# Optimization experiments

Measured on AMD Instinct MI355X. Metric: run time of the kernel, lower is better.

Reference implementation:

```python
import jax, jax.numpy as jnp
import numpy as np

OUTPUT_SIZE = 65
THRESHOLD = 0.2
EPS = 1e-6


def setup_inputs() -> dict:
    key = jax.random.key(0)
    x = jax.random.normal(key, (64, 4, 512), dtype=jnp.float32)
    return {"x": x}


def _valid_mask(x):
    # True from first nonzero to last nonzero along L, per (n, c); all False if row is all-zero.
    N, C, L = x.shape
    nz = x != 0
    any_nz = nz.any(axis=2, keepdims=True)            # [N, C, 1]
    first = jnp.argmax(nz, axis=2)                    # [N, C]
    last = (L - 1) - jnp.argmax(nz[:, :, ::-1], axis=2)
    idx = jnp.arange(L)
    mask = (idx[None, None, :] >= first[:, :, None]) & (idx[None, None, :] <= last[:, :, None])
    return mask & any_nz                              # [N, C, L] bool


def reference(x):
    N, C, L = x.shape
    mask = _valid_mask(x)
    mf = mask.astype(x.dtype)
    cnt = jnp.clip(mf.sum(axis=2), 1, None)           # [N, C]
    mean = (x * mf).sum(axis=2) / cnt                 # [N, C]
    var = (((x * mf - mean[..., None]) ** 2) * mf).sum(axis=2) / cnt
    std = jnp.sqrt(var)                               # [N, C]
    x_norm = (x - mean[..., None]) / jnp.clip(std, EPS, None)[..., None]
    x_norm = jnp.where(mask, x_norm, jnp.zeros((), x.dtype))  # [N, C, L]
    # Recurrence plot: cdist on 1-d points == |x_i - x_j|, thresholded.
    dist = jnp.abs(x_norm[..., :, None] - x_norm[..., None, :])  # [N, C, L, L]
    rp = (dist < THRESHOLD).astype(x.dtype)
    size = min(L, OUTPUT_SIZE)
    out = jnp.zeros((N, C, OUTPUT_SIZE, OUTPUT_SIZE), dtype=x.dtype)
    out = out.at[:, :, :size, :size].set(rp[:, :, :size, :size])
    return out
```

## Files before the change

kernel.cpp:

```cpp
#include <hip/hip_runtime.h>
#include <climits>

#define LROW 512
#define OUT_S 65
#define THRESH 0.2f
#define EPS_F 1e-6f

__global__ __launch_bounds__(256) void rp_kernel(const float* __restrict__ x,
                                                 float* __restrict__ out) {
    const int row = blockIdx.x;
    const int tid = threadIdx.x;
    const float* xr = x + (size_t)row * LROW;

    __shared__ float  xs[LROW];
    __shared__ int    s_lo[256];
    __shared__ int    s_hi[256];
    __shared__ double s_d[256];
    __shared__ float  xn[OUT_S];

    const float v0 = xr[tid];
    const float v1 = xr[tid + 256];
    xs[tid]       = v0;
    xs[tid + 256] = v1;

    int lo = INT_MAX, hi = -1;
    if (v0 != 0.0f) { lo = tid; hi = tid; }
    if (v1 != 0.0f) { lo = min(lo, tid + 256); hi = max(hi, tid + 256); }
    s_lo[tid] = lo;
    s_hi[tid] = hi;
    __syncthreads();
    for (int s = 128; s > 0; s >>= 1) {
        if (tid < s) {
            s_lo[tid] = min(s_lo[tid], s_lo[tid + s]);
            s_hi[tid] = max(s_hi[tid], s_hi[tid + s]);
        }
        __syncthreads();
    }
    const int  first = s_lo[0];
    const int  last  = s_hi[0];
    const bool anyNZ = (last >= 0);
    const float cnt  = anyNZ ? (float)(last - first + 1) : 1.0f;

    double sum = 0.0;
    if (anyNZ) {
        if (tid >= first && tid <= last) sum += (double)v0;
        const int i1 = tid + 256;
        if (i1 >= first && i1 <= last) sum += (double)v1;
    }
    s_d[tid] = sum;
    __syncthreads();
    for (int s = 128; s > 0; s >>= 1) {
        if (tid < s) s_d[tid] += s_d[tid + s];
        __syncthreads();
    }
    const float mean = (float)(s_d[0] / (double)cnt);
    __syncthreads();

    double ss = 0.0;
    if (anyNZ) {
        if (tid >= first && tid <= last) {
            const float d = v0 - mean;
            ss += (double)d * (double)d;
        }
        const int i1 = tid + 256;
        if (i1 >= first && i1 <= last) {
            const float d = v1 - mean;
            ss += (double)d * (double)d;
        }
    }
    s_d[tid] = ss;
    __syncthreads();
    for (int s = 128; s > 0; s >>= 1) {
        if (tid < s) s_d[tid] += s_d[tid + s];
        __syncthreads();
    }
    const float stdv = sqrtf((float)(s_d[0] / (double)cnt));
    const float stdc = fmaxf(stdv, EPS_F);

    if (tid < OUT_S) {
        const bool m = anyNZ && (tid >= first) && (tid <= last);
        xn[tid] = m ? (xs[tid] - mean) / stdc : 0.0f;
    }
    __syncthreads();

    float* orow = out + (size_t)row * (OUT_S * OUT_S);
    #pragma unroll 4
    for (int k = tid; k < OUT_S * OUT_S; k += 256) {
        const int i = k / OUT_S;
        const int j = k - i * OUT_S;
        orow[k] = (fabsf(xn[i] - xn[j]) < THRESH) ? 1.0f : 0.0f;
    }
}

extern "C" void kernel_launch(void* const* d_in, const int* in_sizes, int n_in,
                              void* d_out, int out_size, void* d_ws, size_t ws_size,
                              hipStream_t stream) {
    const float* x  = (const float*)d_in[0];
    float*      out = (float*)d_out;
    const int rows  = in_sizes[0] / LROW;
    rp_kernel<<<rows, 256, 0, stream>>>(x, out);
}
```

Measured before the change: 11.66 us.

## Replace shared-memory tree reductions with wave shuffles and single-pass moments

```diff
diff --git a/kernel.cpp b/kernel.cpp
--- a/kernel.cpp
+++ b/kernel.cpp
@@ -3,6 +3,7 @@
 
 #define LROW 512
 #define OUT_S 65
+#define NOUT (OUT_S * OUT_S)
 #define THRESH 0.2f
 #define EPS_F 1e-6f
 
@@ -12,83 +13,62 @@
     const int tid = threadIdx.x;
     const float* xr = x + (size_t)row * LROW;
 
-    __shared__ float  xs[LROW];
-    __shared__ int    s_lo[256];
-    __shared__ int    s_hi[256];
-    __shared__ double s_d[256];
-    __shared__ float  xn[OUT_S];
-
     const float v0 = xr[tid];
     const float v1 = xr[tid + 256];
-    xs[tid]       = v0;
-    xs[tid + 256] = v1;
 
     int lo = INT_MAX, hi = -1;
     if (v0 != 0.0f) { lo = tid; hi = tid; }
     if (v1 != 0.0f) { lo = min(lo, tid + 256); hi = max(hi, tid + 256); }
-    s_lo[tid] = lo;
-    s_hi[tid] = hi;
-    __syncthreads();
-    for (int s = 128; s > 0; s >>= 1) {
-        if (tid < s) {
-            s_lo[tid] = min(s_lo[tid], s_lo[tid + s]);
-            s_hi[tid] = max(s_hi[tid], s_hi[tid + s]);
-        }
-        __syncthreads();
+    double s1 = (double)v0 + (double)v1;
+    double s2 = (double)v0 * (double)v0 + (double)v1 * (double)v1;
+
+    #pragma unroll
+    for (int off = 32; off > 0; off >>= 1) {
+        lo = min(lo, __shfl_xor(lo, off, 64));
+        hi = max(hi, __shfl_xor(hi, off, 64));
+        s1 += __shfl_xor(s1, off, 64);
+        s2 += __shfl_xor(s2, off, 64);
     }
-    const int  first = s_lo[0];
-    const int  last  = s_hi[0];
-    const bool anyNZ = (last >= 0);
-    const float cnt  = anyNZ ? (float)(last - first + 1) : 1.0f;
 
-    double sum = 0.0;
-    if (anyNZ) {
-        if (tid >= first && tid <= last) sum += (double)v0;
-        const int i1 = tid + 256;
-        if (i1 >= first && i1 <= last) sum += (double)v1;
+    __shared__ int    w_lo[4], w_hi[4];
+    __shared__ double w_s1[4], w_s2[4];
+    __shared__ float  xn[OUT_S];
+
+    const int wid = tid >> 6;
+    if ((tid & 63) == 0) {
+        w_lo[wid] = lo; w_hi[wid] = hi; w_s1[wid] = s1; w_s2[wid] = s2;
     }
-    s_d[tid] = sum;
-    __syncthreads();
-    for (int s = 128; s > 0; s >>= 1) {
-        if (tid < s) s_d[tid] += s_d[tid + s];
-        __syncthreads();
-    }
-    const float mean = (float)(s_d[0] / (double)cnt);
     __syncthreads();
 
-    double ss = 0.0;
-    if (anyNZ) {
-        if (tid >= first && tid <= last) {
-            const float d = v0 - mean;
-            ss += (double)d * (double)d;
-        }
-        const int i1 = tid + 256;
-        if (i1 >= first && i1 <= last) {
-            const float d = v1 - mean;
-            ss += (double)d * (double)d;
-        }
-    }
-    s_d[tid] = ss;
-    __syncthreads();
-    for (int s = 128; s > 0; s >>= 1) {
-        if (tid < s) s_d[tid] += s_d[tid + s];
-        __syncthreads();
-    }
-    const float stdv = sqrtf((float)(s_d[0] / (double)cnt));
-    const float stdc = fmaxf(stdv, EPS_F);
+    const int first = min(min(w_lo[0], w_lo[1]), min(w_lo[2], w_lo[3]));
+    const int last  = max(max(w_hi[0], w_hi[1]), max(w_hi[2], w_hi[3]));
+    const double S1 = (w_s1[0] + w_s1[1]) + (w_s1[2] + w_s1[3]);
+    const double S2 = (w_s2[0] + w_s2[1]) + (w_s2[2] + w_s2[3]);
+
+    const bool   anyNZ = (last >= 0);
+    const double cnt   = anyNZ ? (double)(last - first + 1) : 1.0;
+    const float  mean  = (float)(S1 / cnt);
+    const double dm    = (double)mean;
+    double var = (S2 - 2.0 * dm * S1 + cnt * dm * dm) / cnt;
+    var = var > 0.0 ? var : 0.0;
+    const float stdc = fmaxf(sqrtf((float)var), EPS_F);
 
     if (tid < OUT_S) {
         const bool m = anyNZ && (tid >= first) && (tid <= last);
-        xn[tid] = m ? (xs[tid] - mean) / stdc : 0.0f;
+        xn[tid] = m ? (v0 - mean) / stdc : 0.0f;
     }
     __syncthreads();
 
-    float* orow = out + (size_t)row * (OUT_S * OUT_S);
-    #pragma unroll 4
-    for (int k = tid; k < OUT_S * OUT_S; k += 256) {
-        const int i = k / OUT_S;
-        const int j = k - i * OUT_S;
-        orow[k] = (fabsf(xn[i] - xn[j]) < THRESH) ? 1.0f : 0.0f;
+    float* orow = out + (size_t)row * NOUT;
+    int k = tid;
+    #pragma unroll
+    for (int it = 0; it < 17; ++it) {
+        if (k < NOUT) {
+            const int ii = k / OUT_S;
+            const int jj = k - ii * OUT_S;
+            orow[k] = (fabsf(xn[ii] - xn[jj]) < THRESH) ? 1.0f : 0.0f;
+        }
+        k += 256;
     }
 }
 
```

Result: faster. 10.59 us (-9.2%).
